# Performance work log

Hardware: AMD Instinct MI355X
Metric: run time of the kernel (lower is better)

## Reference

```python
import jax, jax.numpy as jnp
import numpy as np

DIM = 3072
NUM_HEADS = 24
HEAD_DIM = DIM // NUM_HEADS  # 128
SEQ = 2048
BATCH = 1


def rms_norm(x, scale):
    # compute in fp32 like the torch module
    xf = x.astype(jnp.float32)
    rrms = jax.lax.rsqrt(jnp.mean(xf * xf, axis=-1, keepdims=True) + 1e-6)
    return (xf * rrms).astype(x.dtype) * scale


def apply_rope(xq, xk, pe):
    # xq, xk: [B, H, L, D]; pe: [B, 1, L, D//2, 2, 2]
    shp = xq.shape
    xq_ = xq.reshape(*shp[:-1], -1, 1, 2).astype(jnp.float32)
    xk_ = xk.reshape(*shp[:-1], -1, 1, 2).astype(jnp.float32)
    xq_out = pe[..., 0] * xq_[..., 0] + pe[..., 1] * xq_[..., 1]
    xk_out = pe[..., 0] * xk_[..., 0] + pe[..., 1] * xk_[..., 1]
    return xq_out.reshape(shp).astype(xq.dtype), xk_out.reshape(shp).astype(xk.dtype)


def setup_inputs() -> dict:
    key = jax.random.key(0)
    ks = jax.random.split(key, 6)
    s = 1.0 / np.sqrt(DIM)
    return {
        "x": jax.random.normal(ks[0], (BATCH, SEQ, DIM), dtype=jnp.float32),
        "pe": jax.random.normal(ks[1], (BATCH, 1, SEQ, HEAD_DIM // 2, 2, 2), dtype=jnp.float32),
        "w_qkv": jax.random.normal(ks[2], (3 * DIM, DIM), dtype=jnp.float32) * s,
        "w_proj": jax.random.normal(ks[3], (DIM, DIM), dtype=jnp.float32) * s,
        "b_proj": jax.random.normal(ks[4], (DIM,), dtype=jnp.float32) * 0.01,
        "q_scale": jnp.ones((HEAD_DIM,), dtype=jnp.float32),
        "k_scale": jnp.ones((HEAD_DIM,), dtype=jnp.float32),
    }


def reference(x, pe, w_qkv, w_proj, b_proj, q_scale, k_scale):
    B, L, _ = x.shape
    # fused qkv projection (qkv_bias=False)
    qkv = jnp.einsum("bld,ed->ble", x, w_qkv)  # [B, L, 3*DIM]
    qkv = qkv.reshape(B, L, 3, NUM_HEADS, HEAD_DIM)
    qkv = jnp.transpose(qkv, (2, 0, 3, 1, 4))  # [3, B, H, L, D]
    q, k, v = qkv[0], qkv[1], qkv[2]
    # QKNorm (RMSNorm on head_dim)
    q = rms_norm(q, q_scale).astype(v.dtype)
    k = rms_norm(k, k_scale).astype(v.dtype)
    # rope
    q, k = apply_rope(q, k, pe)
    # scaled dot-product attention
    scale = 1.0 / np.sqrt(HEAD_DIM)
    scores = jnp.einsum("bhqd,bhkd->bhqk", q, k) * scale
    probs = jax.nn.softmax(scores, axis=-1)
    out = jnp.einsum("bhqk,bhkd->bhqd", probs, v)
    out = jnp.transpose(out, (0, 2, 1, 3)).reshape(B, L, DIM)  # merge heads
    # output projection
    return jnp.einsum("bld,ed->ble", out, w_proj) + b_proj
```

## Files before the change

kernel.cpp:

```cpp
#include <hip/hip_runtime.h>

typedef __bf16 bf16;
typedef __attribute__((ext_vector_type(8))) __bf16 bf16x8;
typedef __attribute__((ext_vector_type(4))) float f32x4;

typedef __attribute__((address_space(1))) void gvoid_t;
typedef __attribute__((address_space(3))) void lvoid_t;

#define LDS_LOAD16(gp, lp) \
    __builtin_amdgcn_global_load_lds((gvoid_t*)(gp), (lvoid_t*)(lp), 16, 0, 0)

__global__ __launch_bounds__(256)
void f32_to_bf16(const float* __restrict__ in, bf16* __restrict__ out, int n8)
{
    const int i = blockIdx.x * 256 + threadIdx.x;
    if (i >= n8) return;
    const float4 a = ((const float4*)in)[i * 2];
    const float4 b = ((const float4*)in)[i * 2 + 1];
    bf16x8 o;
    o[0] = (bf16)a.x; o[1] = (bf16)a.y; o[2] = (bf16)a.z; o[3] = (bf16)a.w;
    o[4] = (bf16)b.x; o[5] = (bf16)b.y; o[6] = (bf16)b.z; o[7] = (bf16)b.w;
    *(bf16x8*)(out + (size_t)i * 8) = o;
}

template <int BIAS, typename CT>
__global__ __launch_bounds__(256, 2)
void gemm_bt(const bf16* __restrict__ A, const bf16* __restrict__ B,
             const float* __restrict__ bias, CT* __restrict__ C,
             int K, int ldc)
{
    __shared__ bf16 sA[128 * 32];
    __shared__ bf16 sB[128 * 32];
    const int tid  = threadIdx.x;
    const int lane = tid & 63;
    const int wid  = tid >> 6;
    const int m0 = blockIdx.y * 128;
    const int n0 = blockIdx.x * 128;
    const int wm = (wid >> 1) * 64;
    const int wn = (wid & 1) * 64;
    const int l15   = lane & 15;
    const int quad8 = (lane >> 4) * 8;

    f32x4 acc[4][4] = {};

    for (int k0 = 0; k0 < K; k0 += 32) {
#pragma unroll
        for (int t = 0; t < 2; ++t) {
            const int e  = (t * 4 + wid) * 512;
            const int ge = e + lane * 8;
            const int r = ge >> 5, c = ge & 31;
            LDS_LOAD16(A + (size_t)(m0 + r) * K + k0 + c, sA + e);
            LDS_LOAD16(B + (size_t)(n0 + r) * K + k0 + c, sB + e);
        }
        __syncthreads();

        bf16x8 af[4], bfr[4];
#pragma unroll
        for (int i = 0; i < 4; ++i) {
            af[i]  = *(const bf16x8*)(sA + (wm + i * 16 + l15) * 32 + quad8);
            bfr[i] = *(const bf16x8*)(sB + (wn + i * 16 + l15) * 32 + quad8);
        }
#pragma unroll
        for (int i = 0; i < 4; ++i)
#pragma unroll
            for (int j = 0; j < 4; ++j)
                acc[i][j] = __builtin_amdgcn_mfma_f32_16x16x32_bf16(af[i], bfr[j], acc[i][j], 0, 0, 0);
        __syncthreads();
    }

    const int rowBase = m0 + wm + (lane >> 4) * 4;
    const int colBase = n0 + wn + l15;
#pragma unroll
    for (int j = 0; j < 4; ++j) {
        const int col = colBase + j * 16;
        const float bv = BIAS ? bias[col] : 0.0f;
#pragma unroll
        for (int i = 0; i < 4; ++i) {
            const int row = rowBase + i * 16;
#pragma unroll
            for (int r = 0; r < 4; ++r)
                C[(size_t)(row + r) * ldc + col] = (CT)(acc[i][j][r] + bv);
        }
    }
}

__global__ __launch_bounds__(256)
void qk_rope_rearrange(const bf16* __restrict__ qkv, const float* __restrict__ pe,
                       const float* __restrict__ qs, const float* __restrict__ ks,
                       bf16* __restrict__ Qh, bf16* __restrict__ Kh, bf16* __restrict__ Vt)
{
    const int lane = threadIdx.x & 63;
    const int wid  = threadIdx.x >> 6;
    const int idx  = blockIdx.x * 4 + wid;
    const int h = idx >> 11;
    const int l = idx & 2047;

    const size_t rowb = (size_t)l * 9216 + h * 128 + 2 * lane;
    const float q0 = (float)qkv[rowb];
    const float q1 = (float)qkv[rowb + 1];
    const float k0 = (float)qkv[rowb + 3072];
    const float k1 = (float)qkv[rowb + 3073];
    const bf16  v0 = qkv[rowb + 6144];
    const bf16  v1 = qkv[rowb + 6145];

    float ssq = q0 * q0 + q1 * q1;
    float ssk = k0 * k0 + k1 * k1;
#pragma unroll
    for (int off = 1; off < 64; off <<= 1) {
        ssq += __shfl_xor(ssq, off);
        ssk += __shfl_xor(ssk, off);
    }
    const float rq = rsqrtf(ssq * (1.0f / 128.0f) + 1e-6f);
    const float rk = rsqrtf(ssk * (1.0f / 128.0f) + 1e-6f);

    const float s0q = qs[2 * lane], s1q = qs[2 * lane + 1];
    const float s0k = ks[2 * lane], s1k = ks[2 * lane + 1];

    const float qn0 = (q0 * rq) * s0q;
    const float qn1 = (q1 * rq) * s1q;
    const float kn0 = (k0 * rk) * s0k;
    const float kn1 = (k1 * rk) * s1k;

    const float* pp = pe + ((size_t)l * 64 + lane) * 4;
    const float p00 = pp[0], p01 = pp[1];
    const float p10 = pp[2], p11 = pp[3];

    const bf16 qo0 = (bf16)(p00 * qn0 + p01 * qn1);
    const bf16 qo1 = (bf16)(p10 * qn0 + p11 * qn1);
    const bf16 ko0 = (bf16)(p00 * kn0 + p01 * kn1);
    const bf16 ko1 = (bf16)(p10 * kn0 + p11 * kn1);

    const size_t ob = ((size_t)h * 2048 + l) * 128 + 2 * lane;
    Qh[ob] = qo0; Qh[ob + 1] = qo1;
    Kh[ob] = ko0; Kh[ob + 1] = ko1;

    const size_t vb = ((size_t)h * 128 + 2 * lane) * 2048 + l;
    Vt[vb]        = v0;
    Vt[vb + 2048] = v1;
}

__global__ __launch_bounds__(256, 2)
void flash_attn(const bf16* __restrict__ Qh, const bf16* __restrict__ Kh,
                const bf16* __restrict__ Vt, bf16* __restrict__ AO)
{
    __shared__ bf16 sK[2 * 64 * 128];
    __shared__ bf16 sV[2 * 128 * 64];
    __shared__ bf16 sP[4 * 16 * 72];

    const int tid   = threadIdx.x;
    const int lane  = tid & 63;
    const int wid   = tid >> 6;
    const int h     = blockIdx.y;
    const int qw    = blockIdx.x * 64 + wid * 16;
    const int l15   = lane & 15;
    const int quad  = lane >> 4;
    const int quad8 = quad * 8;

    const bf16* Kbase = Kh + (size_t)h * 2048 * 128;
    const bf16* Vbase = Vt + (size_t)h * 128 * 2048;

    bf16x8 aq[4];
    {
        const bf16* qp = Qh + ((size_t)h * 2048 + qw + l15) * 128 + quad8;
#pragma unroll
        for (int ki = 0; ki < 4; ++ki) aq[ki] = *(const bf16x8*)(qp + ki * 32);
    }

    bf16x8 ones;
#pragma unroll
    for (int i = 0; i < 8; ++i) ones[i] = (bf16)1.0f;

    f32x4 o[8] = {};
    f32x4 lacc = {};

    bf16* sPw = sP + wid * (16 * 72);
    const int slotbase = wid * 64;

#define STAGE_K(kv, buf)                                                         \
    {                                                                            \
        bf16* kb = sK + (buf) * (64 * 128);                                      \
        _Pragma("unroll")                                                        \
        for (int t = 0; t < 4; ++t) {                                            \
            const int sb   = t * 256 + slotbase;                                 \
            const int slot = sb + lane;                                          \
            const int r    = slot >> 4;                                          \
            const int cg   = (slot & 15) ^ (r & 7);                              \
            LDS_LOAD16(Kbase + (size_t)((kv) + r) * 128 + cg * 8, kb + sb * 8);  \
        }                                                                        \
    }
#define STAGE_V(kv, buf)                                                         \
    {                                                                            \
        bf16* vb = sV + (buf) * (128 * 64);                                      \
        _Pragma("unroll")                                                        \
        for (int t = 0; t < 4; ++t) {                                            \
            const int sb   = t * 256 + slotbase;                                 \
            const int slot = sb + lane;                                          \
            const int r    = slot >> 3;                                          \
            const int cg   = (slot & 7) ^ (r & 7);                               \
            LDS_LOAD16(Vbase + (size_t)r * 2048 + (kv) + cg * 8, vb + sb * 8);   \
        }                                                                        \
    }

    STAGE_K(0, 0);
    STAGE_V(0, 0);

    for (int s = 0; s < 32; ++s) {
        __syncthreads();
        if (s < 31) {
            STAGE_K((s + 1) * 64, (s + 1) & 1);
            STAGE_V((s + 1) * 64, (s + 1) & 1);
        }

        const bf16* kb = sK + (s & 1) * (64 * 128);
        const bf16* vb = sV + (s & 1) * (128 * 64);

        f32x4 sc[4];
#pragma unroll
        for (int nt = 0; nt < 4; ++nt) {
            f32x4 t = {};
            const int row = nt * 16 + l15;
#pragma unroll
            for (int ki = 0; ki < 4; ++ki) {
                const int pcg = (4 * ki + quad) ^ (l15 & 7);
                bf16x8 bk = *(const bf16x8*)(kb + row * 128 + pcg * 8);
                t = __builtin_amdgcn_mfma_f32_16x16x32_bf16(aq[ki], bk, t, 0, 0, 0);
            }
            sc[nt] = t;
        }

#pragma unroll
        for (int r = 0; r < 4; ++r) {
            const float scl = 0.08838834764831845f;
            bf16* pw = sPw + (quad * 4 + r) * 72 + l15;
            pw[0]  = (bf16)__expf(sc[0][r] * scl);
            pw[16] = (bf16)__expf(sc[1][r] * scl);
            pw[32] = (bf16)__expf(sc[2][r] * scl);
            pw[48] = (bf16)__expf(sc[3][r] * scl);
        }

#pragma unroll
        for (int kk = 0; kk < 2; ++kk) {
            bf16x8 pa = *(const bf16x8*)(sPw + l15 * 72 + kk * 32 + quad8);
            lacc = __builtin_amdgcn_mfma_f32_16x16x32_bf16(pa, ones, lacc, 0, 0, 0);
#pragma unroll
            for (int dt = 0; dt < 8; ++dt) {
                const int row = dt * 16 + l15;
                const int pcg = (kk * 4 + quad) ^ (l15 & 7);
                bf16x8 bv = *(const bf16x8*)(vb + row * 64 + pcg * 8);
                o[dt] = __builtin_amdgcn_mfma_f32_16x16x32_bf16(pa, bv, o[dt], 0, 0, 0);
            }
        }
    }
#undef STAGE_K
#undef STAGE_V

#pragma unroll
    for (int r = 0; r < 4; ++r) {
        const float inv = 1.0f / lacc[r];
        const size_t row = qw + quad * 4 + r;
        bf16* op = AO + row * 3072 + h * 128 + l15;
#pragma unroll
        for (int dt = 0; dt < 8; ++dt) op[dt * 16] = (bf16)(o[dt][r] * inv);
    }
}

extern "C" void kernel_launch(void* const* d_in, const int* in_sizes, int n_in,
                              void* d_out, int out_size, void* d_ws, size_t ws_size,
                              hipStream_t stream)
{
    (void)in_sizes; (void)n_in; (void)out_size;

    const float* x      = (const float*)d_in[0];
    const float* pe     = (const float*)d_in[1];
    const float* w_qkv  = (const float*)d_in[2];
    const float* w_proj = (const float*)d_in[3];
    const float* b_proj = (const float*)d_in[4];
    const float* q_s    = (const float*)d_in[5];
    const float* k_s    = (const float*)d_in[6];
    float* out = (float*)d_out;

    const size_t NEED_BIG = ((size_t)6291456 + 28311552 + 18874368 + 6291456) * 2;

    if (ws_size >= NEED_BIG) {
        bf16* xb  = (bf16*)d_ws;
        bf16* wb  = xb + (size_t)6291456;
        bf16* qkv = wb + (size_t)28311552;
        bf16* Vt  = qkv + (size_t)18874368;
        bf16* Qh  = xb;
        bf16* Kh  = wb;
        bf16* wpb = qkv;
        bf16* AO  = qkv + (size_t)9437184;

        f32_to_bf16<<<dim3(3072),  256, 0, stream>>>(x,     xb, 786432);
        f32_to_bf16<<<dim3(13824), 256, 0, stream>>>(w_qkv, wb, 3538944);
        gemm_bt<0, bf16><<<dim3(72, 16), 256, 0, stream>>>(xb, wb, nullptr, qkv, 3072, 9216);
        qk_rope_rearrange<<<dim3(12288), 256, 0, stream>>>(qkv, pe, q_s, k_s, Qh, Kh, Vt);
        f32_to_bf16<<<dim3(4608), 256, 0, stream>>>(w_proj, wpb, 1179648);
        flash_attn<<<dim3(32, 24), 256, 0, stream>>>(Qh, Kh, Vt, AO);
        gemm_bt<1, float><<<dim3(24, 16), 256, 0, stream>>>(AO, wpb, b_proj, out, 3072, 3072);
    } else {
        bf16* xb  = (bf16*)d_ws;
        bf16* wb  = xb + (size_t)6291456;
        bf16* qkv = wb + (size_t)9437184;
        bf16* Vt  = qkv + (size_t)18874368;
        bf16* Qh  = xb;
        bf16* Kh  = wb;
        bf16* wpb = qkv;
        bf16* AO  = qkv + (size_t)9437184;

        f32_to_bf16<<<dim3(3072), 256, 0, stream>>>(x, xb, 786432);
        for (int c = 0; c < 3; ++c) {
            f32_to_bf16<<<dim3(4608), 256, 0, stream>>>(w_qkv + (size_t)c * 9437184, wb, 1179648);
            gemm_bt<0, bf16><<<dim3(24, 16), 256, 0, stream>>>(xb, wb, nullptr, qkv + c * 3072, 3072, 9216);
        }
        qk_rope_rearrange<<<dim3(12288), 256, 0, stream>>>(qkv, pe, q_s, k_s, Qh, Kh, Vt);
        f32_to_bf16<<<dim3(4608), 256, 0, stream>>>(w_proj, wpb, 1179648);
        flash_attn<<<dim3(32, 24), 256, 0, stream>>>(Qh, Kh, Vt, AO);
        gemm_bt<1, float><<<dim3(24, 16), 256, 0, stream>>>(AO, wpb, b_proj, out, 3072, 3072);
    }
}
```

Measured before the change: 594.3 us.

## Add 256x192 tiled QKV GEMM with phased LDS pipelining and 512 threads

Adds a new bf16 GEMM kernel for the QKV projection that uses 256x192 block tiles, 8 waves, and double-buffered direct-to-LDS loads. Loads are interleaved across four compute phases per k-tile, with swizzled LDS layout and wave priority raised around the MFMA bursts. The aim is more data reuse per loaded tile and better overlap of global loads with matrix math than the previous 128x128 kernel. The cost is more LDS and registers per block, and a grid of 384 blocks, which may fill the CUs less evenly.

Result: faster. 572.3 us (-3.7%).

```diff
diff --git a/kernel.cpp b/kernel.cpp
--- a/kernel.cpp
+++ b/kernel.cpp
@@ -84,6 +84,143 @@
     }
 }
 
+template <int BIAS, typename CT>
+__global__ __launch_bounds__(512, 2)
+void gemm256_bt(const bf16* __restrict__ A, const bf16* __restrict__ B,
+                const float* __restrict__ bias, CT* __restrict__ C,
+                int K, int ldc)
+{
+    __shared__ bf16 sA[2 * 256 * 64];
+    __shared__ bf16 sB[2 * 192 * 64];
+
+    const int tid  = threadIdx.x;
+    const int lane = tid & 63;
+    const int wid  = tid >> 6;
+    const int m0 = blockIdx.y * 256;
+    const int n0 = blockIdx.x * 192;
+    const int wm = (wid >> 2) * 128;
+    const int wn = (wid & 3) * 48;
+    const int l15  = lane & 15;
+    const int quad = lane >> 4;
+    const int swz  = l15 & 7;
+
+    int aoff[4], boff[3];
+    int adst[4], bdst[3];
+#pragma unroll
+    for (int t = 0; t < 4; ++t) {
+        const int slot = t * 512 + tid;
+        const int r  = slot >> 3;
+        const int cg = (slot & 7) ^ (r & 7);
+        aoff[t] = (m0 + r) * K + cg * 8;
+        adst[t] = (t * 512 + wid * 64) * 8;
+    }
+#pragma unroll
+    for (int t = 0; t < 3; ++t) {
+        const int slot = t * 512 + tid;
+        const int r  = slot >> 3;
+        const int cg = (slot & 7) ^ (r & 7);
+        boff[t] = (n0 + r) * K + cg * 8;
+        bdst[t] = (t * 512 + wid * 64) * 8;
+    }
+
+#define STA(t, kt, buf) LDS_LOAD16(A + (size_t)aoff[t] + (kt) * 64, sA + (buf) * 16384 + adst[t])
+#define STB(t, kt, buf) LDS_LOAD16(B + (size_t)boff[t] + (kt) * 64, sB + (buf) * 12288 + bdst[t])
+
+    int aRd[2], bRd[2];
+#pragma unroll
+    for (int kk = 0; kk < 2; ++kk) {
+        const int pcg = (kk * 4 + quad) ^ swz;
+        aRd[kk] = (wm + l15) * 128 + pcg * 16;
+        bRd[kk] = (wn + l15) * 128 + pcg * 16;
+    }
+
+    f32x4 acc[8][3] = {};
+    bf16x8 bfrag[3][2];
+
+#pragma unroll
+    for (int t = 0; t < 3; ++t) STB(t, 0, 0);
+#pragma unroll
+    for (int t = 0; t < 4; ++t) STA(t, 0, 0);
+#pragma unroll
+    for (int t = 0; t < 3; ++t) STB(t, 1, 1);
+    asm volatile("s_waitcnt vmcnt(3)" ::: "memory");
+    __builtin_amdgcn_s_barrier();
+
+#define GRP_PHASE(p, gb, STAGE_STMT, WAITC)                                         \
+    {                                                                               \
+        bf16x8 af[2][2];                                                            \
+        _Pragma("unroll")                                                           \
+        for (int mi = 0; mi < 2; ++mi)                                              \
+            _Pragma("unroll")                                                       \
+            for (int kk = 0; kk < 2; ++kk)                                          \
+                af[mi][kk] = *(const bf16x8*)((const char*)sA + (gb) * 32768 +      \
+                                              aRd[kk] + ((p) * 2 + mi) * 2048);     \
+        if ((p) == 0) {                                                             \
+            _Pragma("unroll")                                                       \
+            for (int nf = 0; nf < 3; ++nf)                                          \
+                _Pragma("unroll")                                                   \
+                for (int kk = 0; kk < 2; ++kk)                                      \
+                    bfrag[nf][kk] = *(const bf16x8*)((const char*)sB + (gb) * 24576 \
+                                                     + bRd[kk] + nf * 2048);        \
+        }                                                                           \
+        STAGE_STMT;                                                                 \
+        __builtin_amdgcn_s_barrier();                                               \
+        asm volatile("s_waitcnt lgkmcnt(0)" ::: "memory");                          \
+        __builtin_amdgcn_sched_barrier(0);                                          \
+        __builtin_amdgcn_s_setprio(1);                                              \
+        _Pragma("unroll")                                                           \
+        for (int mi = 0; mi < 2; ++mi)                                              \
+            _Pragma("unroll")                                                       \
+            for (int nf = 0; nf < 3; ++nf)                                          \
+                _Pragma("unroll")                                                   \
+                for (int kk = 0; kk < 2; ++kk)                                      \
+                    acc[(p) * 2 + mi][nf] = __builtin_amdgcn_mfma_f32_16x16x32_bf16(\
+                        af[mi][kk], bfrag[nf][kk], acc[(p) * 2 + mi][nf], 0, 0, 0); \
+        __builtin_amdgcn_s_setprio(0);                                              \
+        __builtin_amdgcn_sched_barrier(0);                                          \
+        WAITC;                                                                      \
+        __builtin_amdgcn_s_barrier();                                               \
+    }
+
+    const int NT = K >> 6;
+#pragma unroll 1
+    for (int u = 0; u < NT; u += 2) {
+        const int t_o  = u + 1;
+        const int t_e2 = (u + 2 < NT) ? u + 2 : NT - 1;
+        const int t_o2 = (u + 3 < NT) ? u + 3 : NT - 1;
+        GRP_PHASE(0, 0, { STA(0, t_o, 1); STA(1, t_o, 1); }, )
+        GRP_PHASE(1, 0, { STA(2, t_o, 1); STA(3, t_o, 1); }, )
+        GRP_PHASE(2, 0, { STB(0, t_e2, 0); }, )
+        GRP_PHASE(3, 0, { STB(1, t_e2, 0); STB(2, t_e2, 0); },
+                  asm volatile("s_waitcnt vmcnt(3)" ::: "memory"))
+        GRP_PHASE(0, 1, { STA(0, t_e2, 0); STA(1, t_e2, 0); }, )
+        GRP_PHASE(1, 1, { STA(2, t_e2, 0); STA(3, t_e2, 0); }, )
+        GRP_PHASE(2, 1, { STB(0, t_o2, 1); }, )
+        GRP_PHASE(3, 1, { STB(1, t_o2, 1); STB(2, t_o2, 1); },
+                  asm volatile("s_waitcnt vmcnt(3)" ::: "memory"))
+    }
+#undef GRP_PHASE
+#undef STA
+#undef STB
+
+    asm volatile("s_waitcnt vmcnt(0)" ::: "memory");
+
+    const int rowBase = m0 + wm + quad * 4;
+    const int colBase = n0 + wn + l15;
+#pragma unroll
+    for (int nf = 0; nf < 3; ++nf) {
+        const int col = colBase + nf * 16;
+        const float bv = BIAS ? bias[col] : 0.0f;
+#pragma unroll
+        for (int mf = 0; mf < 8; ++mf) {
+            const int row = rowBase + mf * 16;
+#pragma unroll
+            for (int r = 0; r < 4; ++r)
+                C[(size_t)(row + r) * ldc + col] = (CT)(acc[mf][nf][r] + bv);
+        }
+    }
+}
+
 __global__ __launch_bounds__(256)
 void qk_rope_rearrange(const bf16* __restrict__ qkv, const float* __restrict__ pe,
                        const float* __restrict__ qs, const float* __restrict__ ks,
@@ -293,7 +430,7 @@
 
         f32_to_bf16<<<dim3(3072),  256, 0, stream>>>(x,     xb, 786432);
         f32_to_bf16<<<dim3(13824), 256, 0, stream>>>(w_qkv, wb, 3538944);
-        gemm_bt<0, bf16><<<dim3(72, 16), 256, 0, stream>>>(xb, wb, nullptr, qkv, 3072, 9216);
+        gemm256_bt<0, bf16><<<dim3(48, 8), 512, 0, stream>>>(xb, wb, nullptr, qkv, 3072, 9216);
         qk_rope_rearrange<<<dim3(12288), 256, 0, stream>>>(qkv, pe, q_s, k_s, Qh, Kh, Vt);
         f32_to_bf16<<<dim3(4608), 256, 0, stream>>>(w_proj, wpb, 1179648);
         flash_attn<<<dim3(32, 24), 256, 0, stream>>>(Qh, Kh, Vt, AO);
```

## Use 128x192-tile 512-thread double-buffered GEMM for the QKV projection

Applied to the files above, without the earlier changes.

Adds a new bf16 GEMM kernel with 128x192 block tiles, 8 waves, and double-buffered LDS loads issued directly from global memory. It uses XOR-swizzled LDS addressing, split fragment loads interleaved with MFMA via waitcnt and sched barriers, and raised wave priority during the MFMA phase. It replaces the previous 128x128-tile 256-thread GEMM for the QKV projection only, aiming for more operand reuse per block and better load/compute overlap. Cost: higher LDS use per block (80 KB) and more registers per thread, which may limit occupancy.

New measurement: 555.4 us. -6.5%, faster.

```diff
diff --git a/kernel.cpp b/kernel.cpp
--- a/kernel.cpp
+++ b/kernel.cpp
@@ -84,6 +84,141 @@
     }
 }
 
+template <int BIAS, typename CT>
+__global__ __launch_bounds__(512, 4)
+void gemm128_bt(const bf16* __restrict__ A, const bf16* __restrict__ B,
+                const float* __restrict__ bias, CT* __restrict__ C,
+                int K, int ldc)
+{
+    __shared__ bf16 sA[2 * 128 * 64];
+    __shared__ bf16 sB[2 * 192 * 64];
+
+    const int tid  = threadIdx.x;
+    const int lane = tid & 63;
+    const int wid  = tid >> 6;
+    const int m0 = blockIdx.y * 128;
+    const int n0 = blockIdx.x * 192;
+    const int wm = (wid >> 2) * 64;
+    const int wn = (wid & 3) * 48;
+    const int l15  = lane & 15;
+    const int quad = lane >> 4;
+
+    int aoff[2], boff[3];
+    int adst[2], bdst[3];
+#pragma unroll
+    for (int t = 0; t < 2; ++t) {
+        const int slot = t * 512 + tid;
+        const int r  = slot >> 3;
+        const int cg = (slot & 7) ^ (r & 7);
+        aoff[t] = (m0 + r) * K + cg * 8;
+        adst[t] = (t * 512 + wid * 64) * 8;
+    }
+#pragma unroll
+    for (int t = 0; t < 3; ++t) {
+        const int slot = t * 512 + tid;
+        const int r  = slot >> 3;
+        const int cg = (slot & 7) ^ (r & 7);
+        boff[t] = (n0 + r) * K + cg * 8;
+        bdst[t] = (t * 512 + wid * 64) * 8;
+    }
+
+#define STA(t, kt, buf) LDS_LOAD16(A + (size_t)aoff[t] + (kt) * 64, sA + (buf) * 8192  + adst[t])
+#define STB(t, kt, buf) LDS_LOAD16(B + (size_t)boff[t] + (kt) * 64, sB + (buf) * 12288 + bdst[t])
+
+    int aRd[2], bRd[2];
+#pragma unroll
+    for (int kk = 0; kk < 2; ++kk) {
+        const int pcg = (kk * 4 + quad) ^ (l15 & 7);
+        aRd[kk] = (wm + l15) * 128 + pcg * 16;
+        bRd[kk] = (wn + l15) * 128 + pcg * 16;
+    }
+
+    f32x4 acc[4][3] = {};
+
+#pragma unroll
+    for (int t = 0; t < 2; ++t) STA(t, 0, 0);
+#pragma unroll
+    for (int t = 0; t < 3; ++t) STB(t, 0, 0);
+    asm volatile("s_waitcnt vmcnt(0)" ::: "memory");
+
+    const int NT = K >> 6;
+#pragma unroll 1
+    for (int u = 0; u < NT; ++u) {
+        const int b = u & 1;
+        __builtin_amdgcn_s_barrier();
+        if (u + 1 < NT) {
+            STA(0, u + 1, b ^ 1); STA(1, u + 1, b ^ 1);
+            STB(0, u + 1, b ^ 1); STB(1, u + 1, b ^ 1); STB(2, u + 1, b ^ 1);
+        }
+        __builtin_amdgcn_sched_barrier(0);
+
+        bf16x8 af[4][2], bfr[3][2];
+#pragma unroll
+        for (int mi = 0; mi < 2; ++mi)
+#pragma unroll
+            for (int kk = 0; kk < 2; ++kk)
+                af[mi][kk] = *(const bf16x8*)((const char*)sA + b * 16384 +
+                                              aRd[kk] + mi * 2048);
+#pragma unroll
+        for (int nf = 0; nf < 3; ++nf)
+#pragma unroll
+            for (int kk = 0; kk < 2; ++kk)
+                bfr[nf][kk] = *(const bf16x8*)((const char*)sB + b * 24576 +
+                                               bRd[kk] + nf * 2048);
+        __builtin_amdgcn_sched_barrier(0);
+#pragma unroll
+        for (int mi = 2; mi < 4; ++mi)
+#pragma unroll
+            for (int kk = 0; kk < 2; ++kk)
+                af[mi][kk] = *(const bf16x8*)((const char*)sA + b * 16384 +
+                                              aRd[kk] + mi * 2048);
+        __builtin_amdgcn_sched_barrier(0);
+
+        asm volatile("s_waitcnt lgkmcnt(4)" ::: "memory");
+        __builtin_amdgcn_sched_barrier(0);
+        __builtin_amdgcn_s_setprio(1);
+#pragma unroll
+        for (int mi = 0; mi < 2; ++mi)
+#pragma unroll
+            for (int nf = 0; nf < 3; ++nf)
+#pragma unroll
+                for (int kk = 0; kk < 2; ++kk)
+                    acc[mi][nf] = __builtin_amdgcn_mfma_f32_16x16x32_bf16(
+                        af[mi][kk], bfr[nf][kk], acc[mi][nf], 0, 0, 0);
+        __builtin_amdgcn_sched_barrier(0);
+        asm volatile("s_waitcnt lgkmcnt(0)" ::: "memory");
+        __builtin_amdgcn_sched_barrier(0);
+#pragma unroll
+        for (int mi = 2; mi < 4; ++mi)
+#pragma unroll
+            for (int nf = 0; nf < 3; ++nf)
+#pragma unroll
+                for (int kk = 0; kk < 2; ++kk)
+                    acc[mi][nf] = __builtin_amdgcn_mfma_f32_16x16x32_bf16(
+                        af[mi][kk], bfr[nf][kk], acc[mi][nf], 0, 0, 0);
+        __builtin_amdgcn_s_setprio(0);
+        __builtin_amdgcn_sched_barrier(0);
+        asm volatile("s_waitcnt vmcnt(0)" ::: "memory");
+    }
+#undef STA
+#undef STB
+
+    const int rowBase = m0 + wm + quad * 4;
+    const int colBase = n0 + wn + l15;
+#pragma unroll
+    for (int nf = 0; nf < 3; ++nf) {
+        const int col = colBase + nf * 16;
+        const float bv = BIAS ? bias[col] : 0.0f;
+#pragma unroll
+        for (int mf = 0; mf < 4; ++mf) {
+            const int row = rowBase + mf * 16;
+#pragma unroll
+            for (int r = 0; r < 4; ++r)
+                C[(size_t)(row + r) * ldc + col] = (CT)(acc[mf][nf][r] + bv);
+        }
+    }
+}
+
 __global__ __launch_bounds__(256)
 void qk_rope_rearrange(const bf16* __restrict__ qkv, const float* __restrict__ pe,
                        const float* __restrict__ qs, const float* __restrict__ ks,
@@ -293,7 +428,7 @@
 
         f32_to_bf16<<<dim3(3072),  256, 0, stream>>>(x,     xb, 786432);
         f32_to_bf16<<<dim3(13824), 256, 0, stream>>>(w_qkv, wb, 3538944);
-        gemm_bt<0, bf16><<<dim3(72, 16), 256, 0, stream>>>(xb, wb, nullptr, qkv, 3072, 9216);
+        gemm128_bt<0, bf16><<<dim3(48, 16), 512, 0, stream>>>(xb, wb, nullptr, qkv, 3072, 9216);
         qk_rope_rearrange<<<dim3(12288), 256, 0, stream>>>(qkv, pe, q_s, k_s, Qh, Kh, Vt);
         f32_to_bf16<<<dim3(4608), 256, 0, stream>>>(w_proj, wpb, 1179648);
         flash_attn<<<dim3(32, 24), 256, 0, stream>>>(Qh, Kh, Vt, AO);
```
